# Kernel optimization log

Measured on AMD Instinct MI355X. Metric: run time of the kernel, lower is better.

The kernel has to match this reference:

```python
import jax, jax.numpy as jnp
import numpy as np


def setup_inputs() -> dict:
    key = jax.random.key(0)
    k1, k2, k3 = jax.random.split(key, 3)
    B, N, Nq, D, Dv = 32, 4096, 8, 64, 64
    return {
        "keys": jax.random.normal(k1, (B, N, D), dtype=jnp.float32),
        "values": jax.random.normal(k2, (B, N, Dv), dtype=jnp.float32),
        "query": jax.random.normal(k3, (B, Nq, D), dtype=jnp.float32),
    }


def reference(keys, values, query):
    eps = 1e-8
    d = keys.shape[-1]
    # scores: B x N x N'  (same math as broadcast multiply + sum over D)
    alpha = jnp.einsum("bnd,bmd->bnm", keys, query) / jnp.sqrt(jnp.float32(d))
    # softmax over slots (last axis)
    alpha = jax.nn.softmax(alpha, axis=-1) + eps
    # renormalize over input tokens (axis=1)
    alpha = alpha / jnp.sum(alpha, axis=1, keepdims=True)
    # weighted sum of values over N: B x N' x D'
    return jnp.einsum("bnm,bnv->bmv", alpha, values)
```

## Files before the change

### kernel.cpp

```cpp
#include <hip/hip_runtime.h>

#define BB 32
#define NN 4096
#define NQ 8
#define DD 64
#define DV 64
#define CHUNKS 16
#define TOK_PER_BLOCK (NN / CHUNKS)
#define TOK_PER_WAVE (TOK_PER_BLOCK / 4)
#define NGROUP (TOK_PER_WAVE / 8)

template <int CTRL>
__device__ __forceinline__ float dpp_add(float x) {
    union { float f; int i; } in, out;
    in.f = x;
    out.i = __builtin_amdgcn_update_dpp(0, in.i, CTRL, 0xF, 0xF, true);
    return x + out.f;
}
__device__ __forceinline__ float swz16_add(float x) {
    union { float f; int i; } in, out;
    in.f = x;
    out.i = __builtin_amdgcn_ds_swizzle(in.i, 0x401F);
    return x + out.f;
}

__global__ __launch_bounds__(256, 2) void slot_attn_partial(
    const float* __restrict__ keys, const float* __restrict__ values,
    const float* __restrict__ query, float* __restrict__ PU, float* __restrict__ PS)
{
    const int b     = blockIdx.y;
    const int chnk  = blockIdx.x;
    const int tid   = threadIdx.x;
    const int wave  = tid >> 6;
    const int lane  = tid & 63;
    const int t_sub = lane >> 3;
    const int g     = lane & 7;

    float4 q0[8], q1[8];
    const float* qb = query + (size_t)b * NQ * DD + 8 * g;
#pragma unroll
    for (int m = 0; m < 8; ++m) {
        float4 a = *(const float4*)(qb + m * DD);
        float4 c = *(const float4*)(qb + m * DD + 4);
        a.x *= 0.125f; a.y *= 0.125f; a.z *= 0.125f; a.w *= 0.125f;
        c.x *= 0.125f; c.y *= 0.125f; c.z *= 0.125f; c.w *= 0.125f;
        q0[m] = a; q1[m] = c;
    }

    const int tok0 = chnk * TOK_PER_BLOCK + wave * TOK_PER_WAVE;
    const float* Kbase = keys   + ((size_t)b * NN + tok0) * DD + 8 * g;
    const float* Vbase = values + ((size_t)b * NN + tok0) * DV + 8 * g;

    float u[8][8];
#pragma unroll
    for (int m = 0; m < 8; ++m)
#pragma unroll
        for (int j = 0; j < 8; ++j) u[m][j] = 0.f;
    float s_acc[8];
#pragma unroll
    for (int m = 0; m < 8; ++m) s_acc[m] = 0.f;

    float4 kb0[4], kb1[4], vb0[4], vb1[4];
#pragma unroll
    for (int p = 0; p < 3; ++p) {
        const float4* kp = (const float4*)(Kbase + (size_t)(8 * p + t_sub) * DD);
        const float4* vp = (const float4*)(Vbase + (size_t)(8 * p + t_sub) * DV);
        kb0[p] = kp[0]; kb1[p] = kp[1]; vb0[p] = vp[0]; vb1[p] = vp[1];
    }

#pragma unroll
    for (int i = 0; i < NGROUP; ++i) {
        const int cur = i & 3;
        if (i + 3 < NGROUP) {
            const int nxt = (i + 3) & 3;
            const float4* kp = (const float4*)(Kbase + (size_t)(8 * (i + 3) + t_sub) * DD);
            const float4* vp = (const float4*)(Vbase + (size_t)(8 * (i + 3) + t_sub) * DV);
            kb0[nxt] = kp[0]; kb1[nxt] = kp[1]; vb0[nxt] = vp[0]; vb1[nxt] = vp[1];
        }

        const float4 kc0 = kb0[cur], kc1 = kb1[cur];
        float s[8];
#pragma unroll
        for (int m = 0; m < 8; ++m) {
            s[m] = kc0.x * q0[m].x + kc0.y * q0[m].y + kc0.z * q0[m].z + kc0.w * q0[m].w
                 + kc1.x * q1[m].x + kc1.y * q1[m].y + kc1.z * q1[m].z + kc1.w * q1[m].w;
        }
#pragma unroll
        for (int m = 0; m < 8; ++m) {
            s[m] = dpp_add<0xB1>(s[m]);
            s[m] = dpp_add<0x4E>(s[m]);
            s[m] = dpp_add<0x141>(s[m]);
        }
        float e[8], sum = 0.f;
#pragma unroll
        for (int m = 0; m < 8; ++m) { e[m] = __expf(s[m]); sum += e[m]; }
        const float r = __builtin_amdgcn_rcpf(sum);
        const float4 vc0 = vb0[cur], vc1 = vb1[cur];
#pragma unroll
        for (int m = 0; m < 8; ++m) {
            const float a = e[m] * r + 1e-8f;
            s_acc[m] += a;
            u[m][0] += a * vc0.x; u[m][1] += a * vc0.y;
            u[m][2] += a * vc0.z; u[m][3] += a * vc0.w;
            u[m][4] += a * vc1.x; u[m][5] += a * vc1.y;
            u[m][6] += a * vc1.z; u[m][7] += a * vc1.w;
        }
    }

#pragma unroll
    for (int m = 0; m < 8; ++m) {
#pragma unroll
        for (int j = 0; j < 8; ++j) {
            u[m][j] = dpp_add<0x128>(u[m][j]);
            u[m][j] = swz16_add(u[m][j]);
        }
        s_acc[m] = dpp_add<0x128>(s_acc[m]);
        s_acc[m] = swz16_add(s_acc[m]);
    }

    __shared__ float lds[8 * 512];
    __shared__ float lds_s[8 * 8];
    const int half = lane >> 5;
    if ((lane & 24) == 0) {
        float* dst = lds + (wave * 2 + half) * 512 + 8 * g;
#pragma unroll
        for (int m = 0; m < 8; ++m)
#pragma unroll
            for (int j = 0; j < 8; ++j) dst[m * 64 + j] = u[m][j];
        if (g == 0) {
#pragma unroll
            for (int m = 0; m < 8; ++m) lds_s[(wave * 2 + half) * 8 + m] = s_acc[m];
        }
    }
    __syncthreads();

    float* pu = PU + ((size_t)b * CHUNKS + chnk) * 512;
#pragma unroll
    for (int o = 0; o < 2; ++o) {
        int idx = o * 256 + tid;
        float sum = 0.f;
#pragma unroll
        for (int k = 0; k < 8; ++k) sum += lds[k * 512 + idx];
        pu[idx] = sum;
    }
    if (tid < 8) {
        float ssum = 0.f;
#pragma unroll
        for (int k = 0; k < 8; ++k) ssum += lds_s[k * 8 + tid];
        PS[((size_t)b * CHUNKS + chnk) * 8 + tid] = ssum;
    }
}

__global__ __launch_bounds__(512) void slot_attn_reduce(
    const float* __restrict__ PU, const float* __restrict__ PS,
    float* __restrict__ out)
{
    const int b = blockIdx.x;
    const int i = threadIdx.x;

    __shared__ float ssum[NQ];
    if (i < NQ) {
        float s = 0.f;
        const float* ps = PS + (size_t)b * CHUNKS * 8 + i;
#pragma unroll
        for (int c = 0; c < CHUNKS; ++c) s += ps[c * 8];
        ssum[i] = s;
    }
    __syncthreads();

    float usum = 0.f;
    const float* pu = PU + (size_t)b * CHUNKS * 512 + i;
#pragma unroll
    for (int c = 0; c < CHUNKS; ++c) usum += pu[c * 512];
    out[(size_t)b * 512 + i] = usum / ssum[i >> 6];
}

extern "C" void kernel_launch(void* const* d_in, const int* in_sizes, int n_in,
                              void* d_out, int out_size, void* d_ws, size_t ws_size,
                              hipStream_t stream) {
    const float* keys   = (const float*)d_in[0];
    const float* values = (const float*)d_in[1];
    const float* query  = (const float*)d_in[2];
    float* out = (float*)d_out;

    float* PU = (float*)d_ws;
    float* PS = PU + (size_t)BB * CHUNKS * 512;

    slot_attn_partial<<<dim3(CHUNKS, BB), 256, 0, stream>>>(keys, values, query, PU, PS);
    slot_attn_reduce<<<dim3(BB), 512, 0, stream>>>(PU, PS, out);
}
```

Before: 99.57 us.

## Fuse partial and reduce kernels into one block per batch and value half

Replaces the two-kernel scheme (per-chunk partial sums written to workspace, then a reduce kernel) with a single kernel. Each of 64 blocks of 512 threads covers a whole batch over all 4096 tokens but only half of the value dimension. The final normalisation is done in LDS, so the workspace round trip and the second launch go away. Block IDs are remapped so both halves of a batch land on the same XCD and can share keys in L2. The trade-off is heavy: only 64 blocks on a 256-CU GPU, and every key dot product, softmax and exp is computed twice (once per value half), so the kernel likely loses much of its memory-level parallelism.

```diff
diff --git a/kernel.cpp b/kernel.cpp
--- a/kernel.cpp
+++ b/kernel.cpp
@@ -5,9 +5,8 @@
 #define NQ 8
 #define DD 64
 #define DV 64
-#define CHUNKS 16
-#define TOK_PER_BLOCK (NN / CHUNKS)
-#define TOK_PER_WAVE (TOK_PER_BLOCK / 4)
+#define WAVES 8
+#define TOK_PER_WAVE (NN / WAVES)
 #define NGROUP (TOK_PER_WAVE / 8)
 
 template <int CTRL>
@@ -24,12 +23,16 @@
     return x + out.f;
 }
 
-__global__ __launch_bounds__(256, 2) void slot_attn_partial(
+__global__ __launch_bounds__(512, 2) void slot_attn_fused(
     const float* __restrict__ keys, const float* __restrict__ values,
-    const float* __restrict__ query, float* __restrict__ PU, float* __restrict__ PS)
+    const float* __restrict__ query, float* __restrict__ out)
 {
-    const int b     = blockIdx.y;
-    const int chnk  = blockIdx.x;
+    const int id  = blockIdx.x;
+    const int xcd = id & 7;
+    const int k   = id >> 3;
+    const int b   = xcd + ((k >> 1) << 3);
+    const int h   = k & 1;
+
     const int tid   = threadIdx.x;
     const int wave  = tid >> 6;
     const int lane  = tid & 63;
@@ -47,35 +50,35 @@
         q0[m] = a; q1[m] = c;
     }
 
-    const int tok0 = chnk * TOK_PER_BLOCK + wave * TOK_PER_WAVE;
+    const int tok0 = wave * TOK_PER_WAVE;
     const float* Kbase = keys   + ((size_t)b * NN + tok0) * DD + 8 * g;
-    const float* Vbase = values + ((size_t)b * NN + tok0) * DV + 8 * g;
+    const float* Vbase = values + ((size_t)b * NN + tok0) * DV + h * 32 + 4 * g;
 
-    float u[8][8];
+    float u[8][4];
 #pragma unroll
     for (int m = 0; m < 8; ++m)
 #pragma unroll
-        for (int j = 0; j < 8; ++j) u[m][j] = 0.f;
+        for (int j = 0; j < 4; ++j) u[m][j] = 0.f;
     float s_acc[8];
 #pragma unroll
     for (int m = 0; m < 8; ++m) s_acc[m] = 0.f;
 
-    float4 kb0[4], kb1[4], vb0[4], vb1[4];
+    float4 kb0[4], kb1[4], vb[4];
 #pragma unroll
     for (int p = 0; p < 3; ++p) {
         const float4* kp = (const float4*)(Kbase + (size_t)(8 * p + t_sub) * DD);
-        const float4* vp = (const float4*)(Vbase + (size_t)(8 * p + t_sub) * DV);
-        kb0[p] = kp[0]; kb1[p] = kp[1]; vb0[p] = vp[0]; vb1[p] = vp[1];
+        kb0[p] = kp[0]; kb1[p] = kp[1];
+        vb[p]  = *(const float4*)(Vbase + (size_t)(8 * p + t_sub) * DV);
     }
 
-#pragma unroll
+#pragma unroll 4
     for (int i = 0; i < NGROUP; ++i) {
         const int cur = i & 3;
         if (i + 3 < NGROUP) {
             const int nxt = (i + 3) & 3;
             const float4* kp = (const float4*)(Kbase + (size_t)(8 * (i + 3) + t_sub) * DD);
-            const float4* vp = (const float4*)(Vbase + (size_t)(8 * (i + 3) + t_sub) * DV);
-            kb0[nxt] = kp[0]; kb1[nxt] = kp[1]; vb0[nxt] = vp[0]; vb1[nxt] = vp[1];
+            kb0[nxt] = kp[0]; kb1[nxt] = kp[1];
+            vb[nxt]  = *(const float4*)(Vbase + (size_t)(8 * (i + 3) + t_sub) * DV);
         }
 
         const float4 kc0 = kb0[cur], kc1 = kb1[cur];
@@ -95,22 +98,20 @@
 #pragma unroll
         for (int m = 0; m < 8; ++m) { e[m] = __expf(s[m]); sum += e[m]; }
         const float r = __builtin_amdgcn_rcpf(sum);
-        const float4 vc0 = vb0[cur], vc1 = vb1[cur];
+        const float4 vc = vb[cur];
 #pragma unroll
         for (int m = 0; m < 8; ++m) {
             const float a = e[m] * r + 1e-8f;
             s_acc[m] += a;
-            u[m][0] += a * vc0.x; u[m][1] += a * vc0.y;
-            u[m][2] += a * vc0.z; u[m][3] += a * vc0.w;
-            u[m][4] += a * vc1.x; u[m][5] += a * vc1.y;
-            u[m][6] += a * vc1.z; u[m][7] += a * vc1.w;
+            u[m][0] += a * vc.x; u[m][1] += a * vc.y;
+            u[m][2] += a * vc.z; u[m][3] += a * vc.w;
         }
     }
 
 #pragma unroll
     for (int m = 0; m < 8; ++m) {
 #pragma unroll
-        for (int j = 0; j < 8; ++j) {
+        for (int j = 0; j < 4; ++j) {
             u[m][j] = dpp_add<0x128>(u[m][j]);
             u[m][j] = swz16_add(u[m][j]);
         }
@@ -118,15 +119,14 @@
         s_acc[m] = swz16_add(s_acc[m]);
     }
 
-    __shared__ float lds[8 * 512];
-    __shared__ float lds_s[8 * 8];
+    __shared__ float lds[16 * 256];
+    __shared__ float lds_s[16 * 8];
     const int half = lane >> 5;
     if ((lane & 24) == 0) {
-        float* dst = lds + (wave * 2 + half) * 512 + 8 * g;
+        float* dst = lds + (wave * 2 + half) * 256 + 4 * g;
 #pragma unroll
         for (int m = 0; m < 8; ++m)
-#pragma unroll
-            for (int j = 0; j < 8; ++j) dst[m * 64 + j] = u[m][j];
+            *(float4*)(dst + m * 32) = make_float4(u[m][0], u[m][1], u[m][2], u[m][3]);
         if (g == 0) {
 #pragma unroll
             for (int m = 0; m < 8; ++m) lds_s[(wave * 2 + half) * 8 + m] = s_acc[m];
@@ -134,45 +134,16 @@
     }
     __syncthreads();
 
-    float* pu = PU + ((size_t)b * CHUNKS + chnk) * 512;
+    if (tid < 256) {
+        float usum = 0.f;
 #pragma unroll
-    for (int o = 0; o < 2; ++o) {
-        int idx = o * 256 + tid;
-        float sum = 0.f;
-#pragma unroll
-        for (int k = 0; k < 8; ++k) sum += lds[k * 512 + idx];
-        pu[idx] = sum;
-    }
-    if (tid < 8) {
+        for (int p = 0; p < 16; ++p) usum += lds[p * 256 + tid];
+        const int m = tid >> 5;
         float ssum = 0.f;
 #pragma unroll
-        for (int k = 0; k < 8; ++k) ssum += lds_s[k * 8 + tid];
-        PS[((size_t)b * CHUNKS + chnk) * 8 + tid] = ssum;
+        for (int p = 0; p < 16; ++p) ssum += lds_s[p * 8 + m];
+        out[(size_t)b * (NQ * DV) + m * DV + h * 32 + (tid & 31)] = usum / ssum;
     }
-}
-
-__global__ __launch_bounds__(512) void slot_attn_reduce(
-    const float* __restrict__ PU, const float* __restrict__ PS,
-    float* __restrict__ out)
-{
-    const int b = blockIdx.x;
-    const int i = threadIdx.x;
-
-    __shared__ float ssum[NQ];
-    if (i < NQ) {
-        float s = 0.f;
-        const float* ps = PS + (size_t)b * CHUNKS * 8 + i;
-#pragma unroll
-        for (int c = 0; c < CHUNKS; ++c) s += ps[c * 8];
-        ssum[i] = s;
-    }
-    __syncthreads();
-
-    float usum = 0.f;
-    const float* pu = PU + (size_t)b * CHUNKS * 512 + i;
-#pragma unroll
-    for (int c = 0; c < CHUNKS; ++c) usum += pu[c * 512];
-    out[(size_t)b * 512 + i] = usum / ssum[i >> 6];
 }
 
 extern "C" void kernel_launch(void* const* d_in, const int* in_sizes, int n_in,
@@ -181,11 +152,7 @@
     const float* keys   = (const float*)d_in[0];
     const float* values = (const float*)d_in[1];
     const float* query  = (const float*)d_in[2];
-    float* out = (float*)d_out;
+    (void)d_ws; (void)ws_size;
 
-    float* PU = (float*)d_ws;
-    float* PS = PU + (size_t)BB * CHUNKS * 512;
-
-    slot_attn_partial<<<dim3(CHUNKS, BB), 256, 0, stream>>>(keys, values, query, PU, PS);
-    slot_attn_reduce<<<dim3(BB), 512, 0, stream>>>(PU, PS, out);
+    slot_attn_fused<<<dim3(64), 512, 0, stream>>>(keys, values, query, (float*)d_out);
 }
```

Result: slower. 128.3 us (+28.8%).

## Split value dimension across two blocks to double grid and halve registers

Applied to the files above, without the earlier changes.

Each partial block now handles half of the value dimension (32 of 64 columns), doubling the grid to 1024 blocks, and launch bounds are raised to 4 blocks per SM. Keys and scores are recomputed redundantly in both halves, so key traffic and softmax work double. In exchange, the smaller accumulator and value buffers cut register pressure, allowing more occupancy and more parallelism to hide memory latency. The reduce kernel indexing is adjusted to the new partial layout.

```diff
diff --git a/kernel.cpp b/kernel.cpp
--- a/kernel.cpp
+++ b/kernel.cpp
@@ -24,12 +24,13 @@
     return x + out.f;
 }
 
-__global__ __launch_bounds__(256, 2) void slot_attn_partial(
+__global__ __launch_bounds__(256, 4) void slot_attn_partial(
     const float* __restrict__ keys, const float* __restrict__ values,
     const float* __restrict__ query, float* __restrict__ PU, float* __restrict__ PS)
 {
     const int b     = blockIdx.y;
-    const int chnk  = blockIdx.x;
+    const int chnk  = blockIdx.x & 15;
+    const int hb    = blockIdx.x >> 4;
     const int tid   = threadIdx.x;
     const int wave  = tid >> 6;
     const int lane  = tid & 63;
@@ -49,23 +50,23 @@
 
     const int tok0 = chnk * TOK_PER_BLOCK + wave * TOK_PER_WAVE;
     const float* Kbase = keys   + ((size_t)b * NN + tok0) * DD + 8 * g;
-    const float* Vbase = values + ((size_t)b * NN + tok0) * DV + 8 * g;
+    const float* Vbase = values + ((size_t)b * NN + tok0) * DV + hb * 32 + 4 * g;
 
-    float u[8][8];
+    float u[8][4];
 #pragma unroll
     for (int m = 0; m < 8; ++m)
 #pragma unroll
-        for (int j = 0; j < 8; ++j) u[m][j] = 0.f;
+        for (int j = 0; j < 4; ++j) u[m][j] = 0.f;
     float s_acc[8];
 #pragma unroll
     for (int m = 0; m < 8; ++m) s_acc[m] = 0.f;
 
-    float4 kb0[4], kb1[4], vb0[4], vb1[4];
+    float4 kb0[4], kb1[4], vb[4];
 #pragma unroll
     for (int p = 0; p < 3; ++p) {
         const float4* kp = (const float4*)(Kbase + (size_t)(8 * p + t_sub) * DD);
-        const float4* vp = (const float4*)(Vbase + (size_t)(8 * p + t_sub) * DV);
-        kb0[p] = kp[0]; kb1[p] = kp[1]; vb0[p] = vp[0]; vb1[p] = vp[1];
+        kb0[p] = kp[0]; kb1[p] = kp[1];
+        vb[p]  = *(const float4*)(Vbase + (size_t)(8 * p + t_sub) * DV);
     }
 
 #pragma unroll
@@ -74,8 +75,8 @@
         if (i + 3 < NGROUP) {
             const int nxt = (i + 3) & 3;
             const float4* kp = (const float4*)(Kbase + (size_t)(8 * (i + 3) + t_sub) * DD);
-            const float4* vp = (const float4*)(Vbase + (size_t)(8 * (i + 3) + t_sub) * DV);
-            kb0[nxt] = kp[0]; kb1[nxt] = kp[1]; vb0[nxt] = vp[0]; vb1[nxt] = vp[1];
+            kb0[nxt] = kp[0]; kb1[nxt] = kp[1];
+            vb[nxt]  = *(const float4*)(Vbase + (size_t)(8 * (i + 3) + t_sub) * DV);
         }
 
         const float4 kc0 = kb0[cur], kc1 = kb1[cur];
@@ -95,22 +96,20 @@
 #pragma unroll
         for (int m = 0; m < 8; ++m) { e[m] = __expf(s[m]); sum += e[m]; }
         const float r = __builtin_amdgcn_rcpf(sum);
-        const float4 vc0 = vb0[cur], vc1 = vb1[cur];
+        const float4 vc = vb[cur];
 #pragma unroll
         for (int m = 0; m < 8; ++m) {
             const float a = e[m] * r + 1e-8f;
             s_acc[m] += a;
-            u[m][0] += a * vc0.x; u[m][1] += a * vc0.y;
-            u[m][2] += a * vc0.z; u[m][3] += a * vc0.w;
-            u[m][4] += a * vc1.x; u[m][5] += a * vc1.y;
-            u[m][6] += a * vc1.z; u[m][7] += a * vc1.w;
+            u[m][0] += a * vc.x; u[m][1] += a * vc.y;
+            u[m][2] += a * vc.z; u[m][3] += a * vc.w;
         }
     }
 
 #pragma unroll
     for (int m = 0; m < 8; ++m) {
 #pragma unroll
-        for (int j = 0; j < 8; ++j) {
+        for (int j = 0; j < 4; ++j) {
             u[m][j] = dpp_add<0x128>(u[m][j]);
             u[m][j] = swz16_add(u[m][j]);
         }
@@ -118,15 +117,14 @@
         s_acc[m] = swz16_add(s_acc[m]);
     }
 
-    __shared__ float lds[8 * 512];
+    __shared__ float lds[8 * 256];
     __shared__ float lds_s[8 * 8];
     const int half = lane >> 5;
     if ((lane & 24) == 0) {
-        float* dst = lds + (wave * 2 + half) * 512 + 8 * g;
+        float* dst = lds + (wave * 2 + half) * 256 + 4 * g;
 #pragma unroll
         for (int m = 0; m < 8; ++m)
-#pragma unroll
-            for (int j = 0; j < 8; ++j) dst[m * 64 + j] = u[m][j];
+            *(float4*)(dst + m * 32) = make_float4(u[m][0], u[m][1], u[m][2], u[m][3]);
         if (g == 0) {
 #pragma unroll
             for (int m = 0; m < 8; ++m) lds_s[(wave * 2 + half) * 8 + m] = s_acc[m];
@@ -134,16 +132,14 @@
     }
     __syncthreads();
 
-    float* pu = PU + ((size_t)b * CHUNKS + chnk) * 512;
-#pragma unroll
-    for (int o = 0; o < 2; ++o) {
-        int idx = o * 256 + tid;
+    float* pu = PU + (((size_t)b * CHUNKS + chnk) * 2 + hb) * 256;
+    {
         float sum = 0.f;
 #pragma unroll
-        for (int k = 0; k < 8; ++k) sum += lds[k * 512 + idx];
-        pu[idx] = sum;
+        for (int k = 0; k < 8; ++k) sum += lds[k * 256 + tid];
+        pu[tid] = sum;
     }
-    if (tid < 8) {
+    if (hb == 0 && tid < 8) {
         float ssum = 0.f;
 #pragma unroll
         for (int k = 0; k < 8; ++k) ssum += lds_s[k * 8 + tid];
@@ -168,11 +164,15 @@
     }
     __syncthreads();
 
+    const int m  = i >> 6;
+    const int v  = i & 63;
+    const int h  = v >> 5;
+    const int vp = v & 31;
     float usum = 0.f;
-    const float* pu = PU + (size_t)b * CHUNKS * 512 + i;
+    const float* pu = PU + (size_t)b * (CHUNKS * 2 * 256) + h * 256 + m * 32 + vp;
 #pragma unroll
     for (int c = 0; c < CHUNKS; ++c) usum += pu[c * 512];
-    out[(size_t)b * 512 + i] = usum / ssum[i >> 6];
+    out[(size_t)b * 512 + i] = usum / ssum[m];
 }
 
 extern "C" void kernel_launch(void* const* d_in, const int* in_sizes, int n_in,
@@ -184,8 +184,8 @@
     float* out = (float*)d_out;
 
     float* PU = (float*)d_ws;
-    float* PS = PU + (size_t)BB * CHUNKS * 512;
+    float* PS = PU + (size_t)BB * CHUNKS * 2 * 256;
 
-    slot_attn_partial<<<dim3(CHUNKS, BB), 256, 0, stream>>>(keys, values, query, PU, PS);
+    slot_attn_partial<<<dim3(CHUNKS * 2, BB), 256, 0, stream>>>(keys, values, query, PU, PS);
     slot_attn_reduce<<<dim3(BB), 512, 0, stream>>>(PU, PS, out);
 }
```

Result: slower. 114.6 us (+15.1%).
